# Performance work log

Hardware: AMD Instinct MI355X
Metric: run time of the kernel (lower is better)

## Reference

```python
import jax, jax.numpy as jnp
import numpy as np

D_MODEL = 1024
NUM_HEAD = 16
CHUNK = 64
NGROUPS = 2
D_HEAD = D_MODEL // NUM_HEAD
NEG = -1e30


def setup_inputs() -> dict:
    key = jax.random.key(0)
    ks = jax.random.split(key, 4)
    bs, seq = 2, 4096
    proj_dim = 3 * D_MODEL + 2 * NGROUPS * D_HEAD
    hidden = jax.random.normal(ks[0], (bs, seq, D_MODEL), jnp.float32)
    W_in = jax.random.normal(ks[1], (D_MODEL, proj_dim), jnp.float32) * (D_MODEL ** -0.5)
    # torch init: uniform_(1, chunk_size-1) then log
    gate_bias = jnp.log(jax.random.uniform(ks[2], (D_MODEL,), jnp.float32, 1.0, CHUNK - 1.0))
    rms_weight = jnp.ones((D_MODEL,), jnp.float32)
    W_out = jax.random.normal(ks[3], (D_MODEL, D_MODEL), jnp.float32) * (D_MODEL ** -0.5)
    return {"hidden_states": hidden, "rms_weight": rms_weight, "W_in": W_in,
            "gate_bias": gate_bias, "W_out": W_out}


def _scan_op(a, b):
    ga, xa = a
    gb, xb = b
    return gb * ga, gb * xa + xb


def reference(hidden_states, rms_weight, W_in, gate_bias, W_out):
    bs, seq, d = hidden_states.shape
    dh = d // NUM_HEAD
    nc = seq // CHUNK
    scale = dh ** -0.5
    rep = NUM_HEAD // NGROUPS

    shortcut = hidden_states
    # RMSNorm
    h = hidden_states * jax.lax.rsqrt(jnp.mean(hidden_states ** 2, axis=-1, keepdims=True) + 1e-6) * rms_weight
    proj = h @ W_in  # [bs, seq, 3d + 2*ng*dh]
    z, x, g, q, k = jnp.split(proj, [d, 2 * d, 3 * d, 3 * d + NGROUPS * dh], axis=-1)
    z = jax.nn.sigmoid(z)
    g = jax.nn.sigmoid(g + gate_bias)

    # repeat grouped q/k across heads (torch .repeat tiles)
    q = jnp.tile(q, (1, 1, rep))
    k = jnp.tile(k, (1, 1, rep))
    qh = q.reshape(bs, seq, NUM_HEAD, dh).transpose(0, 2, 1, 3)  # [b,h,s,dh]

    xc = x.reshape(bs, nc, CHUNK, d)
    gc = g.reshape(bs, nc, CHUNK, d)
    kc = k.reshape(bs, nc, CHUNK, d)
    g2 = jnp.concatenate([gc, gc], axis=-1)           # g.repeat(1,1,1,2)
    v = (1.0 - g2) * jnp.concatenate([xc, kc], axis=-1)
    # gated linear recurrence within each chunk: y_t = g_t*y_{t-1} + v_t
    _, xk = jax.lax.associative_scan(_scan_op, (g2, v), axis=2)

    intra_x = xk[..., :d].reshape(bs, seq, NUM_HEAD, dh).transpose(0, 2, 1, 3)  # [b,h,s,dh]
    intra_k = xk[..., d:].reshape(bs, seq, NUM_HEAD, dh).transpose(0, 2, 1, 3)

    # one kv per chunk (position 0 of each chunk, per torch [..., ::chunk_size, :])
    chunk_k = intra_k[:, :, ::CHUNK, :]  # [b,h,nc,dh]
    chunk_x = intra_x[:, :, ::CHUNK, :]

    # inter-chunk block-causal attention: query in chunk c attends kv chunks < c
    scores = jnp.einsum('bhsd,bhcd->bhsc', qh, chunk_k) * scale
    allowed = (jnp.arange(seq)[:, None] // CHUNK) > jnp.arange(nc)[None, :]  # [s,nc]
    masked = jnp.where(allowed, scores, NEG)

    # intra lse: per-token self dot product
    intra_lse = jnp.einsum('bhsd,bhsd->bhs', qh, intra_k) * scale

    # fused, numerically-stable version of flex_attention + MergeLastToken
    m = jnp.maximum(jnp.max(masked, axis=-1), intra_lse)  # [b,h,s], finite
    w = jnp.exp(masked - m[..., None])                     # zeros where masked
    intra_w = jnp.exp(intra_lse - m)
    denom = jnp.sum(w, axis=-1) + intra_w
    out = (jnp.einsum('bhsc,bhcd->bhsd', w, chunk_x) + intra_w[..., None] * intra_x) / denom[..., None]

    out = out.transpose(0, 2, 1, 3).reshape(bs, seq, d)
    return (z * out) @ W_out + shortcut
```

## Files before the change

kernel.cpp:

```cpp
#include <hip/hip_runtime.h>
#include <hip/hip_bf16.h>

typedef __bf16 bf16x8 __attribute__((ext_vector_type(8)));
typedef __bf16 bf16x4 __attribute__((ext_vector_type(4)));
typedef float  f32x4  __attribute__((ext_vector_type(4)));

#define DM 1024
#define PD 3328
#define TROWS 8192
#define SEQ 4096

__device__ __forceinline__ float sigmoidf(float x) { return 1.f / (1.f + __expf(-x)); }

__device__ __forceinline__ void gload16(const void* g, void* l) {
  __builtin_amdgcn_global_load_lds(
      (const __attribute__((address_space(1))) void*)g,
      (__attribute__((address_space(3))) void*)l, 16, 0, 0);
}

__global__ __launch_bounds__(256) void prep_kernel(const float* __restrict__ Win,
                                                   __bf16* __restrict__ WinT,
                                                   const float* __restrict__ Wout,
                                                   __bf16* __restrict__ WoutT,
                                                   const float* __restrict__ hidden,
                                                   const float* __restrict__ rmsw,
                                                   __bf16* __restrict__ hbf) {
  const int id = blockIdx.x;
  const int tid = threadIdx.x;
  if (id < 4352) {
    __shared__ float tile[32][33];
    const float* in;  __bf16* out;  int K, N, bx, by;
    if (id < 3328) { in = Win;  out = WinT;  K = DM; N = PD; bx = id % 104; by = id / 104; }
    else           { in = Wout; out = WoutT; K = DM; N = DM; bx = (id - 3328) & 31; by = (id - 3328) >> 5; }
    int n0 = bx * 32, k0 = by * 32;
    int tx = tid & 31, ty = tid >> 5;
    for (int i = ty; i < 32; i += 8) tile[i][tx] = in[(size_t)(k0 + i) * N + n0 + tx];
    __syncthreads();
    for (int i = ty; i < 32; i += 8) out[(size_t)(n0 + i) * K + k0 + tx] = (__bf16)tile[tx][i];
  } else {
    int r = id - 4352;
    float4 v = ((const float4*)(hidden + (size_t)r * DM))[tid];
    float ss = v.x * v.x + v.y * v.y + v.z * v.z + v.w * v.w;
#pragma unroll
    for (int off = 32; off > 0; off >>= 1) ss += __shfl_xor(ss, off);
    __shared__ float wsum[4];
    int lane = tid & 63, wid = tid >> 6;
    if (lane == 0) wsum[wid] = ss;
    __syncthreads();
    float tot = wsum[0] + wsum[1] + wsum[2] + wsum[3];
    float inv = rsqrtf(tot * (1.f / 1024.f) + 1e-6f);
    float4 wl = ((const float4*)rmsw)[tid];
    bf16x4 o;
    o[0] = (__bf16)(v.x * inv * wl.x);
    o[1] = (__bf16)(v.y * inv * wl.y);
    o[2] = (__bf16)(v.z * inv * wl.z);
    o[3] = (__bf16)(v.w * inv * wl.w);
    *(bf16x4*)(hbf + (size_t)r * DM + tid * 4) = o;
  }
}

template <int GN, int EPI>
__global__ __launch_bounds__(512, 4) void gemm2p(
    const __bf16* __restrict__ A, const __bf16* __restrict__ Bt,
    int N_out, int K,
    const float* __restrict__ gate_bias, const float* __restrict__ shortcut,
    float* __restrict__ outf, __bf16* __restrict__ zbf, __bf16* __restrict__ xbf,
    __bf16* __restrict__ gbf, __bf16* __restrict__ qbf, __bf16* __restrict__ kbf) {
  __shared__ __bf16 As[2][128 * 64];
  __shared__ __bf16 Bs[2][128 * 64];

  const int tid = threadIdx.x;
  const int lane = tid & 63, wid = tid >> 6;
  const int wr = wid >> 1, wc = wid & 1;

  const int nwg = gridDim.x;
  const int cpx = nwg >> 3;
  const int swz = (blockIdx.x & 7) * cpx + (blockIdx.x >> 3);
  const int ntx = N_out >> 7;
  const int ngn = ntx / GN;
  const int g = swz / (8 * GN), l = swz % (8 * GN);
  const int gm = g / ngn, gn = g % ngn;
  const int m0 = (gm * 8 + (l & 7)) << 7;
  const int n0 = (gn * GN + (l >> 3)) << 7;

  f32x4 acc[2][4] = {};
  const int NT = K >> 6;

  const int arow0 = wr * 32 + (lane & 15);
  const int brow0 = wc * 64 + (lane & 15);

  auto stage = [&](const __bf16* src, int row0, int kt, __bf16* lbuf) {
#pragma unroll
    for (int j = 0; j < 2; ++j) {
      int off16 = tid + j * 512;
      int row = off16 >> 3, slot = off16 & 7;
      int col = (slot ^ (row & 7)) << 3;
      gload16(&src[(size_t)(row0 + row) * K + kt + col], lbuf + off16 * 8);
    }
  };
  auto fragrd = [&](const __bf16* buf, int row, int ks) -> bf16x8 {
    int s = ((ks << 2) + (lane >> 4)) ^ (row & 7);
    return *(const bf16x8*)&buf[(row << 6) + (s << 3)];
  };

  stage(A, m0, 0, &As[0][0]);
  stage(Bt, n0, 0, &Bs[0][0]);
  asm volatile("s_waitcnt vmcnt(0)" ::: "memory");
  __builtin_amdgcn_s_barrier();

  for (int t = 0; t < NT; ++t) {
    const __bf16* Ap = &As[t & 1][0];
    const __bf16* Bp = &Bs[t & 1][0];
    if (t + 1 < NT) {
      stage(A, m0, (t + 1) << 6, &As[(t + 1) & 1][0]);
      stage(Bt, n0, (t + 1) << 6, &Bs[(t + 1) & 1][0]);
    }
#pragma unroll
    for (int ks = 0; ks < 2; ++ks) {
      bf16x8 af[2], bf[4];
#pragma unroll
      for (int m = 0; m < 2; ++m) af[m] = fragrd(Ap, arow0 + m * 16, ks);
#pragma unroll
      for (int n = 0; n < 4; ++n) bf[n] = fragrd(Bp, brow0 + n * 16, ks);
      __builtin_amdgcn_s_setprio(1);
#pragma unroll
      for (int m = 0; m < 2; ++m)
#pragma unroll
        for (int n = 0; n < 4; ++n)
          acc[m][n] = __builtin_amdgcn_mfma_f32_16x16x32_bf16(af[m], bf[n], acc[m][n], 0, 0, 0);
      __builtin_amdgcn_s_setprio(0);
    }
    asm volatile("s_waitcnt vmcnt(0)" ::: "memory");
    __builtin_amdgcn_s_barrier();
  }

#pragma unroll
  for (int m = 0; m < 2; ++m) {
#pragma unroll
    for (int n = 0; n < 4; ++n) {
#pragma unroll
      for (int i = 0; i < 4; ++i) {
        int r = m0 + wr * 32 + m * 16 + ((lane >> 4) << 2) + i;
        int c = n0 + wc * 64 + n * 16 + (lane & 15);
        float v = acc[m][n][i];
        if (EPI == 1) {
          if (c < 1024)       zbf[(size_t)r * DM + c] = (__bf16)sigmoidf(v);
          else if (c < 2048)  xbf[(size_t)r * DM + (c - 1024)] = (__bf16)v;
          else if (c < 3072)  gbf[(size_t)r * DM + (c - 2048)] = (__bf16)sigmoidf(v + gate_bias[c - 2048]);
          else if (c < 3200)  qbf[(size_t)r * 128 + (c - 3072)] = (__bf16)v;
          else                kbf[(size_t)r * 128 + (c - 3200)] = (__bf16)v;
        } else {
          outf[(size_t)r * DM + c] = v + shortcut[(size_t)r * DM + c];
        }
      }
    }
  }
}

__global__ __launch_bounds__(256) void scan_kernel(const __bf16* __restrict__ g,
                                                   const __bf16* __restrict__ x,
                                                   const __bf16* __restrict__ kin,
                                                   __bf16* __restrict__ ixa,
                                                   __bf16* __restrict__ ika,
                                                   __bf16* __restrict__ cxtg) {
  int bx = blockIdx.x;
  int part = bx & 3;
  int c = (bx >> 2) & 63;
  int b = bx >> 8;
  int d = part * 256 + threadIdx.x;
  size_t base = (size_t)b * SEQ + (size_t)c * 64;
  float sx = 0.f, sk = 0.f;
  for (int t = 0; t < 64; ++t) {
    size_t row = base + t;
    float gg = (float)g[row * DM + d];
    float xv = (float)x[row * DM + d];
    float kv = (float)kin[row * 128 + (d & 127)];
    sx = gg * (sx - xv) + xv;
    sk = gg * (sk - kv) + kv;
    ixa[row * DM + d] = (__bf16)sx;
    ika[row * DM + d] = (__bf16)sk;
    if (t == 0) cxtg[((size_t)b * DM + d) * 64 + c] = (__bf16)sx;
  }
}

__global__ __launch_bounds__(256) void attn_kernel(const __bf16* __restrict__ qbf,
                                                   const __bf16* __restrict__ ixa,
                                                   const __bf16* __restrict__ ika,
                                                   const __bf16* __restrict__ cxtg,
                                                   const __bf16* __restrict__ zbf,
                                                   __bf16* __restrict__ y) {
  const int qt = blockIdx.x;
  const int h  = blockIdx.y;
  const int b  = blockIdx.z;
  const int tid = threadIdx.x;
  const int lane = tid & 63, wd = tid >> 6;

  __shared__ __bf16 qs[64 * 72];
  __shared__ __bf16 ck[64 * 72];
  __shared__ __bf16 cxT[64 * 72];
  __shared__ __bf16 pb[64 * 72];
  __shared__ float sc[64 * 65];
  __shared__ float rden[64], iwd[64], rlse[64];

  const size_t base = (size_t)b * SEQ;

  for (int i = tid; i < 512; i += 256) {
    int row = i >> 3, part = i & 7;
    *(bf16x8*)&qs[row * 72 + part * 8] =
        *(const bf16x8*)&qbf[(base + qt * 64 + row) * 128 + (h & 1) * 64 + part * 8];
    *(bf16x8*)&ck[row * 72 + part * 8] =
        *(const bf16x8*)&ika[(base + (size_t)row * 64) * DM + h * 64 + part * 8];
    *(bf16x8*)&cxT[row * 72 + part * 8] =
        *(const bf16x8*)&cxtg[((size_t)b * DM + h * 64 + row) * 64 + part * 8];
  }
  __syncthreads();

  {
    f32x4 d4[4] = {};
#pragma unroll
    for (int kk = 0; kk < 64; kk += 32) {
      bf16x8 a = *(const bf16x8*)&qs[(wd * 16 + (lane & 15)) * 72 + kk + (lane >> 4) * 8];
#pragma unroll
      for (int ni = 0; ni < 4; ++ni) {
        bf16x8 bb = *(const bf16x8*)&ck[(ni * 16 + (lane & 15)) * 72 + kk + (lane >> 4) * 8];
        d4[ni] = __builtin_amdgcn_mfma_f32_16x16x32_bf16(a, bb, d4[ni], 0, 0, 0);
      }
    }
#pragma unroll
    for (int ni = 0; ni < 4; ++ni)
#pragma unroll
      for (int i = 0; i < 4; ++i) {
        int qrow = wd * 16 + (lane >> 4) * 4 + i;
        int c = ni * 16 + (lane & 15);
        sc[qrow * 65 + c] = 0.125f * d4[ni][i];
      }
  }

  {
    int s = tid >> 2, p = tid & 3;
    const __bf16* krow = &ika[(base + qt * 64 + s) * DM + h * 64 + p * 16];
    float dot = 0.f;
#pragma unroll
    for (int half = 0; half < 2; ++half) {
      bf16x8 qa = *(const bf16x8*)&qs[s * 72 + p * 16 + half * 8];
      bf16x8 ka = *(const bf16x8*)&krow[half * 8];
#pragma unroll
      for (int e = 0; e < 8; ++e) dot += (float)qa[e] * (float)ka[e];
    }
    dot += __shfl_xor(dot, 1);
    dot += __shfl_xor(dot, 2);
    if (p == 0) rlse[s] = 0.125f * dot;
  }
  __syncthreads();

  {
    int s = tid >> 2, p = tid & 3;
    float lse = rlse[s];
    float m = -1e30f;
#pragma unroll
    for (int k = 0; k < 16; ++k) {
      int c = p * 16 + k;
      if (c < qt) m = fmaxf(m, sc[s * 65 + c]);
    }
    m = fmaxf(m, __shfl_xor(m, 1));
    m = fmaxf(m, __shfl_xor(m, 2));
    m = fmaxf(m, lse);
    float den = 0.f;
    bf16x8 w0, w1;
#pragma unroll
    for (int k = 0; k < 16; ++k) {
      int c = p * 16 + k;
      float wv = (c < qt) ? __expf(sc[s * 65 + c] - m) : 0.f;
      if (k < 8) w0[k] = (__bf16)wv; else w1[k - 8] = (__bf16)wv;
      den += wv;
    }
    *(bf16x8*)&pb[s * 72 + p * 16] = w0;
    *(bf16x8*)&pb[s * 72 + p * 16 + 8] = w1;
    den += __shfl_xor(den, 1);
    den += __shfl_xor(den, 2);
    float iw = __expf(lse - m);
    if (p == 0) {
      rden[s] = 1.f / (den + iw);
      iwd[s] = iw;
    }
  }
  __syncthreads();

  {
    f32x4 d4[4] = {};
#pragma unroll
    for (int kk = 0; kk < 64; kk += 32) {
      bf16x8 a = *(const bf16x8*)&pb[(wd * 16 + (lane & 15)) * 72 + kk + (lane >> 4) * 8];
#pragma unroll
      for (int ni = 0; ni < 4; ++ni) {
        bf16x8 bb = *(const bf16x8*)&cxT[(ni * 16 + (lane & 15)) * 72 + kk + (lane >> 4) * 8];
        d4[ni] = __builtin_amdgcn_mfma_f32_16x16x32_bf16(a, bb, d4[ni], 0, 0, 0);
      }
    }
#pragma unroll
    for (int ni = 0; ni < 4; ++ni)
#pragma unroll
      for (int i = 0; i < 4; ++i) {
        int qrow = wd * 16 + (lane >> 4) * 4 + i;
        int j = ni * 16 + (lane & 15);
        size_t srow = base + qt * 64 + qrow;
        float ix = (float)ixa[srow * DM + h * 64 + j];
        float outv = (d4[ni][i] + iwd[qrow] * ix) * rden[qrow];
        float zv = (float)zbf[srow * DM + h * 64 + j];
        y[srow * DM + h * 64 + j] = (__bf16)(outv * zv);
      }
  }
}

extern "C" void kernel_launch(void* const* d_in, const int* in_sizes, int n_in,
                              void* d_out, int out_size, void* d_ws, size_t ws_size,
                              hipStream_t stream) {
  const float* hidden = (const float*)d_in[0];
  const float* rmsw   = (const float*)d_in[1];
  const float* Win    = (const float*)d_in[2];
  const float* gbias  = (const float*)d_in[3];
  const float* Wout   = (const float*)d_in[4];
  float* out = (float*)d_out;

  char* ws = (char*)d_ws;
  size_t o = 0;
  auto alloc = [&](size_t bytes) { char* p = ws + o; o += (bytes + 255) & ~(size_t)255; return p; };
  __bf16* WinT  = (__bf16*)alloc((size_t)PD * DM * 2);
  __bf16* WoutT = (__bf16*)alloc((size_t)DM * DM * 2);
  __bf16* hy    = (__bf16*)alloc((size_t)TROWS * DM * 2);
  __bf16* zbf   = (__bf16*)alloc((size_t)TROWS * DM * 2);
  __bf16* xbf   = (__bf16*)alloc((size_t)TROWS * DM * 2);
  __bf16* gbf   = (__bf16*)alloc((size_t)TROWS * DM * 2);
  __bf16* qbf   = (__bf16*)alloc((size_t)TROWS * 128 * 2);
  __bf16* kbf   = (__bf16*)alloc((size_t)TROWS * 128 * 2);
  __bf16* ixa   = (__bf16*)alloc((size_t)TROWS * DM * 2);
  __bf16* ika   = (__bf16*)alloc((size_t)TROWS * DM * 2);
  __bf16* cxtg  = (__bf16*)alloc((size_t)2 * DM * 64 * 2);

  prep_kernel<<<dim3(12544), 256, 0, stream>>>(Win, WinT, Wout, WoutT, hidden, rmsw, hy);
  gemm2p<13, 1><<<dim3((TROWS / 128) * (PD / 128)), 512, 0, stream>>>(
      hy, WinT, PD, DM, gbias, nullptr, nullptr, zbf, xbf, gbf, qbf, kbf);
  scan_kernel<<<512, 256, 0, stream>>>(gbf, xbf, kbf, ixa, ika, cxtg);
  attn_kernel<<<dim3(64, 16, 2), 256, 0, stream>>>(qbf, ixa, ika, cxtg, zbf, hy);
  gemm2p<8, 0><<<dim3((TROWS / 128) * (DM / 128)), 512, 0, stream>>>(
      hy, WoutT, DM, DM, nullptr, hidden, out, nullptr, nullptr, nullptr, nullptr, nullptr);
}
```

Before: 169.9 us.

## Add 256x128 tile input-projection GEMM with K=32 stages and grouped swizzle

Adds a new GEMM kernel for the input projection that uses 256x128 output tiles with a 32-wide K step, double-buffered LDS loads with XOR swizzle, and a 4x13 grouped block ordering. Each wave computes a 64x64 sub-tile with 16 MFMAs per K step. The goal is more reuse of each loaded tile and fewer workgroups, so global and LDS traffic per FLOP drops. The cost is a barrier every 32 of K and a larger accumulator per wave, which may hurt occupancy.

```diff
diff --git a/kernel.cpp b/kernel.cpp
--- a/kernel.cpp
+++ b/kernel.cpp
@@ -59,6 +59,109 @@
   }
 }
 
+template <int GM, int GN, int EPI>
+__global__ __launch_bounds__(512, 4) void gemm21(
+    const __bf16* __restrict__ A, const __bf16* __restrict__ Bt,
+    int N_out, int K,
+    const float* __restrict__ gate_bias, const float* __restrict__ shortcut,
+    float* __restrict__ outf, __bf16* __restrict__ zbf, __bf16* __restrict__ xbf,
+    __bf16* __restrict__ gbf, __bf16* __restrict__ qbf, __bf16* __restrict__ kbf) {
+  __shared__ __bf16 As[2][256 * 32];
+  __shared__ __bf16 Bs[2][128 * 32];
+
+  const int tid = threadIdx.x;
+  const int lane = tid & 63, wid = tid >> 6;
+  const int wm = wid >> 1, wn = wid & 1;
+  const int lr = lane & 15, hh = lane >> 4;
+
+  const int nwg = gridDim.x, cpx = nwg >> 3;
+  const int swz = (blockIdx.x & 7) * cpx + (blockIdx.x >> 3);
+  const int ntx = N_out >> 7;
+  const int ngn = ntx / GN;
+  const int g = swz / (GM * GN), l = swz % (GM * GN);
+  const int gm = g / ngn, gn = g % ngn;
+  const int m0 = (gm * GM + (l % GM)) << 8;
+  const int n0 = (gn * GN + (l / GM)) << 7;
+
+  f32x4 acc[4][4] = {};
+  const int NT = K >> 5;
+
+  const int arow0 = wm * 64 + lr;
+  const int brow0 = wn * 64 + lr;
+
+  auto stageA = [&](int kt, __bf16* lbuf) {
+#pragma unroll
+    for (int j = 0; j < 2; ++j) {
+      int c = tid + j * 512;
+      int row = c >> 2, s = c & 3;
+      int lsw = s ^ ((row >> 1) & 3);
+      gload16(&A[(size_t)(m0 + row) * K + kt + lsw * 8], lbuf + c * 8);
+    }
+  };
+  auto stageB = [&](int kt, __bf16* lbuf) {
+    int c = tid;
+    int row = c >> 2, s = c & 3;
+    int lsw = s ^ ((row >> 1) & 3);
+    gload16(&Bt[(size_t)(n0 + row) * K + kt + lsw * 8], lbuf + c * 8);
+  };
+  auto fragrd = [&](const __bf16* buf, int row) -> bf16x8 {
+    int s = hh ^ ((row >> 1) & 3);
+    return *(const bf16x8*)&buf[(row << 5) + (s << 3)];
+  };
+
+  stageA(0, &As[0][0]);
+  stageB(0, &Bs[0][0]);
+  asm volatile("s_waitcnt vmcnt(0)" ::: "memory");
+  __builtin_amdgcn_s_barrier();
+
+  for (int t = 0; t < NT; ++t) {
+    const __bf16* Ap = &As[t & 1][0];
+    const __bf16* Bp = &Bs[t & 1][0];
+    if (t + 1 < NT) {
+      stageA((t + 1) << 5, &As[(t + 1) & 1][0]);
+      stageB((t + 1) << 5, &Bs[(t + 1) & 1][0]);
+    }
+    {
+      bf16x8 af[4], bf[4];
+#pragma unroll
+      for (int m = 0; m < 4; ++m) af[m] = fragrd(Ap, arow0 + m * 16);
+#pragma unroll
+      for (int n = 0; n < 4; ++n) bf[n] = fragrd(Bp, brow0 + n * 16);
+      __builtin_amdgcn_s_setprio(1);
+#pragma unroll
+      for (int m = 0; m < 4; ++m)
+#pragma unroll
+        for (int n = 0; n < 4; ++n)
+          acc[m][n] = __builtin_amdgcn_mfma_f32_16x16x32_bf16(af[m], bf[n], acc[m][n], 0, 0, 0);
+      __builtin_amdgcn_s_setprio(0);
+    }
+    asm volatile("s_waitcnt vmcnt(0)" ::: "memory");
+    __builtin_amdgcn_s_barrier();
+  }
+
+#pragma unroll
+  for (int m = 0; m < 4; ++m) {
+#pragma unroll
+    for (int n = 0; n < 4; ++n) {
+#pragma unroll
+      for (int i = 0; i < 4; ++i) {
+        int r = m0 + wm * 64 + m * 16 + (hh << 2) + i;
+        int c = n0 + wn * 64 + n * 16 + lr;
+        float v = acc[m][n][i];
+        if (EPI == 1) {
+          if (c < 1024)       zbf[(size_t)r * DM + c] = (__bf16)sigmoidf(v);
+          else if (c < 2048)  xbf[(size_t)r * DM + (c - 1024)] = (__bf16)v;
+          else if (c < 3072)  gbf[(size_t)r * DM + (c - 2048)] = (__bf16)sigmoidf(v + gate_bias[c - 2048]);
+          else if (c < 3200)  qbf[(size_t)r * 128 + (c - 3072)] = (__bf16)v;
+          else                kbf[(size_t)r * 128 + (c - 3200)] = (__bf16)v;
+        } else {
+          outf[(size_t)r * DM + c] = v + shortcut[(size_t)r * DM + c];
+        }
+      }
+    }
+  }
+}
+
 template <int GN, int EPI>
 __global__ __launch_bounds__(512, 4) void gemm2p(
     const __bf16* __restrict__ A, const __bf16* __restrict__ Bt,
@@ -338,7 +441,7 @@
   __bf16* cxtg  = (__bf16*)alloc((size_t)2 * DM * 64 * 2);
 
   prep_kernel<<<dim3(12544), 256, 0, stream>>>(Win, WinT, Wout, WoutT, hidden, rmsw, hy);
-  gemm2p<13, 1><<<dim3((TROWS / 128) * (PD / 128)), 512, 0, stream>>>(
+  gemm21<4, 13, 1><<<dim3(832), 512, 0, stream>>>(
       hy, WinT, PD, DM, gbias, nullptr, nullptr, zbf, xbf, gbf, qbf, kbf);
   scan_kernel<<<512, 256, 0, stream>>>(gbf, xbf, kbf, ixa, ika, cxtg);
   attn_kernel<<<dim3(64, 16, 2), 256, 0, stream>>>(qbf, ixa, ika, cxtg, zbf, hy);
```

New measurement: 166.4 us (median of 3 runs). 1.02x faster.
